# Kernel optimization log

Measured on AMD Instinct MI355X. Metric: run time of the kernel, lower is better.

Reference implementation:

```python
import jax, jax.numpy as jnp
import numpy as np

TEMP = 1.0  # composition softmax temperature

def _bank_topk(x, U, V, logits, top_k):
    # softmax over primitive logits, select top-k, renormalize, fused low-rank projection
    w = jax.nn.softmax(logits / TEMP)                     # [P]
    tw, ti = jax.lax.top_k(w, top_k)                      # [k], [k]
    tw = tw / tw.sum()
    Us = U[ti]                                            # [k, d_in, r]
    Vs = V[ti]                                            # [k, r, d_out]
    h = jnp.einsum('bsd,kdr->bksr', x, Us)                # low-rank bottleneck
    return jnp.einsum('bksr,kro,k->bso', h, Vs, tw)       # weighted fuse

def reference(x, q_U, q_V, k_U, k_V, v_U, v_V, q_logits, k_logits, v_logits, out_w, top_k):
    B, S, _ = x.shape
    H, D = 16, 64
    q = _bank_topk(x, q_U, q_V, q_logits, top_k)
    k = _bank_topk(x, k_U, k_V, k_logits, top_k)
    v = _bank_topk(x, v_U, v_V, v_logits, top_k)
    q = q.reshape(B, S, H, D).transpose(0, 2, 1, 3)       # [B,H,S,D]
    k = k.reshape(B, S, H, D).transpose(0, 2, 1, 3)
    v = v.reshape(B, S, H, D).transpose(0, 2, 1, 3)
    scale = 1.0 / jnp.sqrt(jnp.asarray(D, dtype=x.dtype))
    scores = jnp.einsum('bhqd,bhkd->bhqk', q, k) * scale  # [B,H,S,S]
    causal = jnp.triu(jnp.ones((S, S), dtype=bool), 1)
    scores = jnp.where(causal[None, None], jnp.finfo(x.dtype).min, scores)
    probs = jax.nn.softmax(scores, axis=-1)
    out = jnp.einsum('bhqk,bhkd->bhqd', probs, v)
    out = out.transpose(0, 2, 1, 3).reshape(B, S, H * D)
    return out @ out_w.T                                   # nn.Linear(H*D, d_model, bias=False)

def setup_inputs() -> dict:
    key = jax.random.key(0)
    ks = jax.random.split(key, 11)
    P, d, r = 16, 1024, 64
    B, S = 4, 1024
    f = jnp.float32
    inp = {
        'x': jax.random.normal(ks[0], (B, S, d), f),
        'q_U': jax.random.normal(ks[1], (P, d, r), f) * (1.0 / np.sqrt(d)),
        'q_V': jax.random.normal(ks[2], (P, r, d), f) * (1.0 / np.sqrt(r)),
        'k_U': jax.random.normal(ks[3], (P, d, r), f) * (1.0 / np.sqrt(d)),
        'k_V': jax.random.normal(ks[4], (P, r, d), f) * (1.0 / np.sqrt(r)),
        'v_U': jax.random.normal(ks[5], (P, d, r), f) * (1.0 / np.sqrt(d)),
        'v_V': jax.random.normal(ks[6], (P, r, d), f) * (1.0 / np.sqrt(r)),
        'q_logits': jax.random.normal(ks[7], (P,), f) * 0.01,
        'k_logits': jax.random.normal(ks[8], (P,), f) * 0.01,
        'v_logits': jax.random.normal(ks[9], (P,), f) * 0.01,
        'out_w': jax.random.normal(ks[10], (d, d), f) * (1.0 / np.sqrt(d)),
        'top_k': 4,
    }
    return inp
```

## Files before the change

kernel.cpp:

```cpp
#include <hip/hip_runtime.h>
#include <math.h>

#define D_MODEL 1024
#define RANK    64
#define PMAX    16
#define S_LEN   1024
#define HD      64
#define MROWS   4096
#define NHEAD   16
#define BATCH   4
#define KCMAX   (PMAX * RANK)

typedef short short8v __attribute__((ext_vector_type(8)));
typedef float floatx4 __attribute__((ext_vector_type(4)));

typedef __attribute__((address_space(1))) const unsigned int* gptr_t;
typedef __attribute__((address_space(3))) unsigned int* lptr_t;

static __device__ __forceinline__ void async16(const void* g, void* l) {
    __builtin_amdgcn_global_load_lds((gptr_t)g, (lptr_t)l, 16, 0, 0);
}

static __device__ __forceinline__ short f2bf(float f) {
    unsigned int u = __float_as_uint(f);
    u = (u + 0x7fffu + ((u >> 16) & 1u)) >> 16;
    return (short)u;
}

__global__ void topk_weights_kernel(const float* __restrict__ ql,
                                    const float* __restrict__ kl,
                                    const float* __restrict__ vl,
                                    const int* __restrict__ topk,
                                    int* __restrict__ idx_out,
                                    float* __restrict__ w_out) {
    int bank = threadIdx.x;
    if (bank >= 3) return;
    const float* lg = (bank == 0) ? ql : (bank == 1) ? kl : vl;
    int K = *topk; if (K < 1) K = 1; if (K > PMAX) K = PMAX;
    float l[PMAX];
    for (int i = 0; i < PMAX; ++i) l[i] = lg[i];
    bool used[PMAX];
    for (int i = 0; i < PMAX; ++i) used[i] = false;
    int   sel_i[PMAX];
    float sel_l[PMAX];
    for (int j = 0; j < K; ++j) {
        int best = -1; float bv = -INFINITY;
        for (int i = 0; i < PMAX; ++i)
            if (!used[i] && l[i] > bv) { bv = l[i]; best = i; }
        used[best] = true; sel_i[j] = best; sel_l[j] = bv;
    }
    float mx = sel_l[0];
    float e[PMAX];
    float sum = 0.f;
    for (int j = 0; j < K; ++j) { e[j] = __expf(sel_l[j] - mx); sum += e[j]; }
    float inv = 1.f / sum;
    for (int j = 0; j < PMAX; ++j) {
        idx_out[bank * PMAX + j] = (j < K) ? sel_i[j] : 0;
        w_out[bank * PMAX + j]   = (j < K) ? e[j] * inv : 0.f;
    }
}

__global__ __launch_bounds__(256) void convert_bf16_kernel(
    const float* __restrict__ src, short* __restrict__ dst, int n4) {
    int i = blockIdx.x * 256 + threadIdx.x;
    if (i < n4) {
        float4 f = ((const float4*)src)[i];
        short4 o;
        o.x = f2bf(f.x); o.y = f2bf(f.y); o.z = f2bf(f.z); o.w = f2bf(f.w);
        ((short4*)dst)[i] = o;
    }
}

__global__ __launch_bounds__(256) void prep_uv_kernel(
    const float* __restrict__ qU, const float* __restrict__ kU,
    const float* __restrict__ vU,
    const float* __restrict__ qV, const float* __restrict__ kV,
    const float* __restrict__ vV,
    const int* __restrict__ idx, const float* __restrict__ wsel,
    const int* __restrict__ topk,
    short* __restrict__ Uc, short* __restrict__ Vt) {
    int z    = blockIdx.z;
    int j    = blockIdx.y;
    int tile = blockIdx.x;
    int t    = threadIdx.x;
    int K = *topk; if (K < 1) K = 1; if (K > PMAX) K = PMAX;
    if (j >= K) return;
    __shared__ float T[64][65];
    int bank = (z < 3) ? z : z - 3;
    int p = idx[bank * PMAX + j];

    if (z < 3) {
        const float* U = (bank == 0) ? qU : (bank == 1) ? kU : vU;
        const float* src = U + (size_t)p * D_MODEL * RANK;
        short* dst = Uc + (size_t)bank * D_MODEL * KCMAX;
        int r4 = (t & 15) * 4;
        int dl = t >> 4;
#pragma unroll
        for (int i = 0; i < 4; ++i) {
            int d = tile * 64 + i * 16 + dl;
            float4 f = *(const float4*)&src[(size_t)d * RANK + r4];
            short4 o;
            o.x = f2bf(f.x); o.y = f2bf(f.y); o.z = f2bf(f.z); o.w = f2bf(f.w);
            *(short4*)&dst[(size_t)d * KCMAX + j * 64 + r4] = o;
        }
    } else {
        const float* V = (bank == 0) ? qV : (bank == 1) ? kV : vV;
        float wj = wsel[bank * PMAX + j];
        const float* src = V + (size_t)p * RANK * D_MODEL;
        int n0 = tile * 64;
        int nl = t & 63, rq = t >> 6;
#pragma unroll
        for (int i = 0; i < 16; ++i) {
            int rl = i * 4 + rq;
            T[nl][rl] = src[(size_t)rl * D_MODEL + n0 + nl] * wj;
        }
        __syncthreads();
        short* dst = Vt + (size_t)bank * D_MODEL * KCMAX;
        int rr = t >> 2;
#pragma unroll
        for (int i = 0; i < 4; ++i) {
            int c = (t & 3) * 16 + i * 4;
            short4 o;
            o.x = f2bf(T[rr][c + 0]); o.y = f2bf(T[rr][c + 1]);
            o.z = f2bf(T[rr][c + 2]); o.w = f2bf(T[rr][c + 3]);
            *(short4*)&dst[(size_t)(n0 + rr) * KCMAX + j * 64 + c] = o;
        }
    }
}

static __device__ __forceinline__ void mfma_gemm_tile(
    const short* __restrict__ A, const short* __restrict__ B, int kl,
    int lda, int ldb, int m0, int n0, short* As, short* Bs, floatx4 acc[4][4]) {
    const int t    = threadIdx.x;
    const int w    = t >> 6;
    const int lane = t & 63;
    const int wm   = w & 1, wn = w >> 1;
    const int colL = lane & 15, quad = lane >> 4;
    const int srow  = lane >> 2;
    const int skoff = (lane & 3) * 8;

#pragma unroll
    for (int i = 0; i < 4; ++i)
#pragma unroll
        for (int j = 0; j < 4; ++j) acc[i][j] = (floatx4){0.f, 0.f, 0.f, 0.f};

    for (int k0 = 0; k0 < kl; k0 += 32) {
        async16(A + (size_t)(m0 + w * 16 + srow) * lda + k0 + skoff,
                As + (w * 16 + srow) * 32 + skoff);
        async16(A + (size_t)(m0 + 64 + w * 16 + srow) * lda + k0 + skoff,
                As + (64 + w * 16 + srow) * 32 + skoff);
        async16(B + (size_t)(n0 + w * 16 + srow) * ldb + k0 + skoff,
                Bs + (w * 16 + srow) * 32 + skoff);
        async16(B + (size_t)(n0 + 64 + w * 16 + srow) * ldb + k0 + skoff,
                Bs + (64 + w * 16 + srow) * 32 + skoff);
        __syncthreads();
        short8v af[4], bf[4];
#pragma unroll
        for (int i = 0; i < 4; ++i)
            af[i] = *(const short8v*)&As[(wm * 64 + i * 16 + colL) * 32 + quad * 8];
#pragma unroll
        for (int j = 0; j < 4; ++j)
            bf[j] = *(const short8v*)&Bs[(wn * 64 + j * 16 + colL) * 32 + quad * 8];
#pragma unroll
        for (int i = 0; i < 4; ++i)
#pragma unroll
            for (int j = 0; j < 4; ++j)
                acc[i][j] = __builtin_amdgcn_mfma_f32_16x16x32_bf16(af[i], bf[j], acc[i][j], 0, 0, 0);
        __syncthreads();
    }
}

__global__ __launch_bounds__(256) void gemm_weff_kernel(
    const short* __restrict__ Vt, const short* __restrict__ Uc,
    const int* __restrict__ topk, short* __restrict__ Wt) {
    int K = *topk; if (K < 1) K = 1; if (K > PMAX) K = PMAX;
    int id = blockIdx.x + 8 * (blockIdx.y + 8 * blockIdx.z);
    int sw = (id & 7) * 24 + (id >> 3);
    int m0 = (sw & 7) * 128; int rest = sw >> 3;
    int n0 = (rest & 7) * 128; int bank = rest >> 3;
    __shared__ short As[128 * 32];
    __shared__ short Bs[128 * 32];
    floatx4 acc[4][4];
    mfma_gemm_tile(Vt + (size_t)bank * D_MODEL * KCMAX,
                   Uc + (size_t)bank * D_MODEL * KCMAX,
                   K * 64, KCMAX, KCMAX, m0, n0, As, Bs, acc);

    const int t = threadIdx.x, w = t >> 6, lane = t & 63;
    const int wm = w & 1, wn = w >> 1, colL = lane & 15, quad = lane >> 4;
    short* Wb = Wt + (size_t)bank * D_MODEL * D_MODEL;
#pragma unroll
    for (int i = 0; i < 4; ++i)
#pragma unroll
        for (int j = 0; j < 4; ++j)
#pragma unroll
            for (int r = 0; r < 4; ++r)
                Wb[(size_t)(m0 + wm * 64 + i * 16 + quad * 4 + r) * D_MODEL +
                   (n0 + wn * 64 + j * 16 + colL)] = f2bf(acc[i][j][r]);
}

__global__ __launch_bounds__(256) void gemm_qkv_kernel(
    const short* __restrict__ xb, const short* __restrict__ Wt,
    short* __restrict__ qkv) {
    int id = blockIdx.x + 32 * (blockIdx.y + 8 * blockIdx.z);
    int sw = (id & 7) * 96 + (id >> 3);
    int m0 = (sw & 31) * 128; int rest = sw >> 5;
    int n0 = (rest & 7) * 128; int bank = rest >> 3;
    __shared__ short As[128 * 32];
    __shared__ short Bs[128 * 32];
    floatx4 acc[4][4];
    mfma_gemm_tile(xb, Wt + (size_t)bank * D_MODEL * D_MODEL,
                   D_MODEL, D_MODEL, D_MODEL, m0, n0, As, Bs, acc);

    const int t = threadIdx.x, w = t >> 6, lane = t & 63;
    const int wm = w & 1, wn = w >> 1, colL = lane & 15, quad = lane >> 4;
    short* outp = qkv + (size_t)bank * MROWS * D_MODEL;
#pragma unroll
    for (int i = 0; i < 4; ++i)
#pragma unroll
        for (int j = 0; j < 4; ++j)
#pragma unroll
            for (int r = 0; r < 4; ++r) {
                int m = m0 + wm * 64 + i * 16 + quad * 4 + r;
                int n = n0 + wn * 64 + j * 16 + colL;
                int b = m >> 10, s = m & 1023;
                int head = n >> 6, d = n & 63;
                outp[(((size_t)(b * NHEAD + head) << 10) + s) * HD + d] = f2bf(acc[i][j][r]);
            }
}

__global__ __launch_bounds__(256) void gemm_proj_kernel(
    const short* __restrict__ attnb, const short* __restrict__ wb,
    float* __restrict__ outp) {
    int id = blockIdx.x + 32 * blockIdx.y;
    int sw = (id & 7) * 32 + (id >> 3);
    int m0 = (sw & 31) * 128;
    int n0 = (sw >> 5) * 128;
    __shared__ short As[128 * 32];
    __shared__ short Bs[128 * 32];
    floatx4 acc[4][4];
    mfma_gemm_tile(attnb, wb, D_MODEL, D_MODEL, D_MODEL, m0, n0, As, Bs, acc);

    const int t = threadIdx.x, w = t >> 6, lane = t & 63;
    const int wm = w & 1, wn = w >> 1, colL = lane & 15, quad = lane >> 4;
#pragma unroll
    for (int i = 0; i < 4; ++i)
#pragma unroll
        for (int j = 0; j < 4; ++j)
#pragma unroll
            for (int r = 0; r < 4; ++r)
                outp[(size_t)(m0 + wm * 64 + i * 16 + quad * 4 + r) * D_MODEL +
                     (n0 + wn * 64 + j * 16 + colL)] = acc[i][j][r];
}

__global__ __launch_bounds__(256) void attn_mfma_kernel(
    const short* __restrict__ qkv,
    short* __restrict__ attn_out) {
    const int t    = threadIdx.x;
    const int w    = t >> 6;
    const int lane = t & 63;
    const int col  = lane & 15;
    const int quad = lane >> 4;
    int id = blockIdx.x + 8 * blockIdx.y;
    int sw = (id & 7) * 64 + (id >> 3);
    const int pr = sw & 7;
    const int bh = sw >> 3;
    const size_t HS   = (size_t)S_LEN * HD;
    const size_t BSTR = (size_t)MROWS * D_MODEL;
    const short* Qg = qkv + (size_t)bh * HS;
    const short* Kg = qkv + BSTR + (size_t)bh * HS;
    const short* Vg = qkv + 2 * BSTR + (size_t)bh * HS;

    __shared__ short Ks[128][72];
    __shared__ short Vt[64][136];
    __shared__ short Ps[4][16][136];

    const float SC = 0.125f * 1.44269504f;

    for (int ph = 0; ph < 2; ++ph) {
        const int qt = ph ? (15 - pr) : pr;
        const int qb = qt * 4 + w;
        const int qrow = qt * 64 + w * 16 + col;
        short8v aq0 = *(const short8v*)(Qg + (size_t)qrow * HD + quad * 8);
        short8v aq1 = *(const short8v*)(Qg + (size_t)qrow * HD + 32 + quad * 8);
        floatx4 O0 = {0.f, 0.f, 0.f, 0.f}, O1 = O0, O2 = O0, O3 = O0;
        float mrow[4] = {-INFINITY, -INFINITY, -INFINITY, -INFINITY};
        float lrow[4] = {0.f, 0.f, 0.f, 0.f};
        const int nkv = (qt + 2) >> 1;

        for (int jt = 0; jt < nkv; ++jt) {
            __syncthreads();
#pragma unroll
            for (int it = 0; it < 4; ++it) {
                int idx = t + it * 256;
                int key = idx >> 3, db = (idx & 7) * 8;
                *(short8v*)&Ks[key][db] =
                    *(const short8v*)(Kg + (size_t)(jt * 128 + key) * HD + db);
            }
#pragma unroll
            for (int it = 0; it < 2; ++it) {
                int idx = t + it * 256;
                int k0 = (idx & 63) * 2;
                int db = (idx >> 6) * 8;
                short8v v0 = *(const short8v*)(Vg + (size_t)(jt * 128 + k0) * HD + db);
                short8v v1 = *(const short8v*)(Vg + (size_t)(jt * 128 + k0 + 1) * HD + db);
#pragma unroll
                for (int i = 0; i < 8; ++i) {
                    unsigned int pk = (unsigned int)(unsigned short)v0[i] |
                                      ((unsigned int)(unsigned short)v1[i] << 16);
                    *(unsigned int*)&Vt[db + i][k0] = pk;
                }
            }
            __syncthreads();

            float sc[8][4];
            const int base = jt * 8;
#pragma unroll
            for (int n = 0; n < 8; ++n) {
                int rel = qb - (base + n);
                if (rel >= 0) {
                    floatx4 c4 = {0.f, 0.f, 0.f, 0.f};
                    short8v b0 = *(const short8v*)&Ks[n * 16 + col][quad * 8];
                    short8v b1 = *(const short8v*)&Ks[n * 16 + col][32 + quad * 8];
                    c4 = __builtin_amdgcn_mfma_f32_16x16x32_bf16(aq0, b0, c4, 0, 0, 0);
                    c4 = __builtin_amdgcn_mfma_f32_16x16x32_bf16(aq1, b1, c4, 0, 0, 0);
#pragma unroll
                    for (int r = 0; r < 4; ++r) {
                        float v = c4[r] * SC;
                        if (rel == 0 && col > quad * 4 + r) v = -INFINITY;
                        sc[n][r] = v;
                    }
                } else {
#pragma unroll
                    for (int r = 0; r < 4; ++r) sc[n][r] = -INFINITY;
                }
            }
#pragma unroll
            for (int r = 0; r < 4; ++r) {
                float tm = sc[0][r];
#pragma unroll
                for (int n = 1; n < 8; ++n) tm = fmaxf(tm, sc[n][r]);
                tm = fmaxf(tm, __shfl_xor(tm, 1));
                tm = fmaxf(tm, __shfl_xor(tm, 2));
                tm = fmaxf(tm, __shfl_xor(tm, 4));
                tm = fmaxf(tm, __shfl_xor(tm, 8));
                if (__any(tm > mrow[r] + 8.0f)) {
                    float mnew  = fmaxf(mrow[r], tm);
                    float alpha = exp2f(mrow[r] - mnew);
                    lrow[r] *= alpha;
                    O0[r] *= alpha; O1[r] *= alpha; O2[r] *= alpha; O3[r] *= alpha;
                    mrow[r] = mnew;
                }
                float ps = 0.f;
#pragma unroll
                for (int n = 0; n < 8; ++n) {
                    float p = exp2f(sc[n][r] - mrow[r]);
                    ps += p;
                    Ps[w][quad * 4 + r][n * 16 + col] = f2bf(p);
                }
                ps += __shfl_xor(ps, 1);
                ps += __shfl_xor(ps, 2);
                ps += __shfl_xor(ps, 4);
                ps += __shfl_xor(ps, 8);
                lrow[r] += ps;
            }
            int lim = qb * 16 + 15 - (jt << 7);
            int ksm = lim >> 5; if (ksm > 3) ksm = 3;
#pragma unroll
            for (int ks = 0; ks < 4; ++ks) {
                if (ks > ksm) break;
                short8v ap  = *(const short8v*)&Ps[w][col][ks * 32 + quad * 8];
                short8v bv0 = *(const short8v*)&Vt[0  + col][ks * 32 + quad * 8];
                short8v bv1 = *(const short8v*)&Vt[16 + col][ks * 32 + quad * 8];
                short8v bv2 = *(const short8v*)&Vt[32 + col][ks * 32 + quad * 8];
                short8v bv3 = *(const short8v*)&Vt[48 + col][ks * 32 + quad * 8];
                O0 = __builtin_amdgcn_mfma_f32_16x16x32_bf16(ap, bv0, O0, 0, 0, 0);
                O1 = __builtin_amdgcn_mfma_f32_16x16x32_bf16(ap, bv1, O1, 0, 0, 0);
                O2 = __builtin_amdgcn_mfma_f32_16x16x32_bf16(ap, bv2, O2, 0, 0, 0);
                O3 = __builtin_amdgcn_mfma_f32_16x16x32_bf16(ap, bv3, O3, 0, 0, 0);
            }
        }
        const int b  = bh >> 4;
        const int hh = bh & 15;
        short* orow = attn_out +
            ((size_t)(b * S_LEN) + qt * 64 + w * 16) * D_MODEL + hh * 64;
#pragma unroll
        for (int r = 0; r < 4; ++r) {
            float inv = 1.f / lrow[r];
            short* prw = orow + (size_t)(quad * 4 + r) * D_MODEL;
            prw[0  + col] = f2bf(O0[r] * inv);
            prw[16 + col] = f2bf(O1[r] * inv);
            prw[32 + col] = f2bf(O2[r] * inv);
            prw[48 + col] = f2bf(O3[r] * inv);
        }
    }
}

extern "C" void kernel_launch(void* const* d_in, const int* in_sizes, int n_in,
                              void* d_out, int out_size, void* d_ws, size_t ws_size,
                              hipStream_t stream) {
    const float* x    = (const float*)d_in[0];
    const float* qU   = (const float*)d_in[1];
    const float* qV   = (const float*)d_in[2];
    const float* kU   = (const float*)d_in[3];
    const float* kV   = (const float*)d_in[4];
    const float* vU   = (const float*)d_in[5];
    const float* vV   = (const float*)d_in[6];
    const float* qlg  = (const float*)d_in[7];
    const float* klg  = (const float*)d_in[8];
    const float* vlg  = (const float*)d_in[9];
    const float* outw = (const float*)d_in[10];
    const int*   topk = (const int*)d_in[11];
    float* outp = (float*)d_out;

    char* ws = (char*)d_ws;
    int*   idxp = (int*)ws;
    float* wp   = (float*)(ws + 256);
    short* xb   = (short*)(ws + 512);
    short* Uc   = xb + (size_t)MROWS * D_MODEL;
    short* Vt   = Uc + (size_t)3 * D_MODEL * KCMAX;
    short* wb   = Vt + (size_t)3 * D_MODEL * KCMAX;
    short* Wt   = wb + (size_t)D_MODEL * D_MODEL;
    short* qkvb = Wt + (size_t)3 * D_MODEL * D_MODEL;
    short* attnb = qkvb + (size_t)3 * MROWS * D_MODEL;

    topk_weights_kernel<<<1, 64, 0, stream>>>(qlg, klg, vlg, topk, idxp, wp);
    convert_bf16_kernel<<<(MROWS * D_MODEL / 4 + 255) / 256, 256, 0, stream>>>(
        x, xb, MROWS * D_MODEL / 4);
    convert_bf16_kernel<<<(D_MODEL * D_MODEL / 4 + 255) / 256, 256, 0, stream>>>(
        outw, wb, D_MODEL * D_MODEL / 4);
    prep_uv_kernel<<<dim3(16, 16, 6), 256, 0, stream>>>(
        qU, kU, vU, qV, kV, vV, idxp, wp, topk, Uc, Vt);
    gemm_weff_kernel<<<dim3(8, 8, 3), 256, 0, stream>>>(Vt, Uc, topk, Wt);
    gemm_qkv_kernel<<<dim3(32, 8, 3), 256, 0, stream>>>(xb, Wt, qkvb);
    attn_mfma_kernel<<<dim3(8, 64), 256, 0, stream>>>(qkvb, attnb);
    gemm_proj_kernel<<<dim3(32, 8), 256, 0, stream>>>(attnb, wb, outp);
}
```

Baseline: 222.8 us.

## Restructure attention kernel with transposed S, async LDS loads, and transpose reads

The attention kernel now computes S^T (keys as MFMA rows), so the softmax probabilities already sit in registers in the layout needed as the A operand for the PV product, removing the Ps LDS round-trip. K and V tiles are loaded with global_load_lds async copies into swizzled layouts, and V is read with ds_read_b64_tr_b16 transpose reads instead of being transposed manually by scalar LDS stores. Row statistics become per-lane scalars, reduced across quads and broadcast with shuffles. This trades more complex indexing and inline asm waits for fewer LDS writes and less VALU work.

Measured after the change: 211.9 us. 4.9% less time.

```diff
diff --git a/kernel.cpp b/kernel.cpp
--- a/kernel.cpp
+++ b/kernel.cpp
@@ -12,10 +12,12 @@
 #define KCMAX   (PMAX * RANK)
 
 typedef short short8v __attribute__((ext_vector_type(8)));
+typedef short short4v __attribute__((ext_vector_type(4)));
 typedef float floatx4 __attribute__((ext_vector_type(4)));
 
 typedef __attribute__((address_space(1))) const unsigned int* gptr_t;
 typedef __attribute__((address_space(3))) unsigned int* lptr_t;
+typedef __attribute__((address_space(3))) short* lds3s;
 
 static __device__ __forceinline__ void async16(const void* g, void* l) {
     __builtin_amdgcn_global_load_lds((gptr_t)g, (lptr_t)l, 16, 0, 0);
@@ -261,20 +263,33 @@
     const int col  = lane & 15;
     const int quad = lane >> 4;
     int id = blockIdx.x + 8 * blockIdx.y;
-    int sw = (id & 7) * 64 + (id >> 3);
-    const int pr = sw & 7;
-    const int bh = sw >> 3;
+    int swz = (id & 7) * 64 + (id >> 3);
+    const int pr = swz & 7;
+    const int bh = swz >> 3;
     const size_t HS   = (size_t)S_LEN * HD;
     const size_t BSTR = (size_t)MROWS * D_MODEL;
     const short* Qg = qkv + (size_t)bh * HS;
     const short* Kg = qkv + BSTR + (size_t)bh * HS;
     const short* Vg = qkv + 2 * BSTR + (size_t)bh * HS;
 
-    __shared__ short Ks[128][72];
-    __shared__ short Vt[64][136];
-    __shared__ short Ps[4][16][136];
+    __shared__ short Ks[128 * 64];
+    __shared__ short Vs[128 * 64];
 
     const float SC = 0.125f * 1.44269504f;
+
+    int krow[4], kslot[4], vkey[4], voff[4];
+#pragma unroll
+    for (int it = 0; it < 4; ++it) {
+        int c = t + it * 256;
+        krow[it]  = c >> 3;
+        kslot[it] = (c & 7) ^ ((c >> 3) & 7);
+        int h = c & 1, kr = (c >> 1) & 3, k4 = (c >> 3) & 31, d16 = c >> 8;
+        vkey[it] = k4 * 4 + kr;
+        voff[it] = d16 * 16 + h * 8;
+    }
+    const int sw0 = (quad ^ (col & 7)) * 16;
+    const int sw1 = ((4 + quad) ^ (col & 7)) * 16;
+    lds3s vb = (lds3s)&Vs[quad * 64 + col * 4];
 
     for (int ph = 0; ph < 2; ++ph) {
         const int qt = ph ? (15 - pr) : pr;
@@ -283,109 +298,115 @@
         short8v aq0 = *(const short8v*)(Qg + (size_t)qrow * HD + quad * 8);
         short8v aq1 = *(const short8v*)(Qg + (size_t)qrow * HD + 32 + quad * 8);
         floatx4 O0 = {0.f, 0.f, 0.f, 0.f}, O1 = O0, O2 = O0, O3 = O0;
-        float mrow[4] = {-INFINITY, -INFINITY, -INFINITY, -INFINITY};
-        float lrow[4] = {0.f, 0.f, 0.f, 0.f};
+        float mrow = -INFINITY, lrow = 0.f;
         const int nkv = (qt + 2) >> 1;
 
         for (int jt = 0; jt < nkv; ++jt) {
             __syncthreads();
 #pragma unroll
             for (int it = 0; it < 4; ++it) {
-                int idx = t + it * 256;
-                int key = idx >> 3, db = (idx & 7) * 8;
-                *(short8v*)&Ks[key][db] =
-                    *(const short8v*)(Kg + (size_t)(jt * 128 + key) * HD + db);
+                async16(Kg + (size_t)(jt * 128 + krow[it]) * HD + kslot[it] * 8,
+                        Ks + (t + it * 256) * 8);
+                async16(Vg + (size_t)(jt * 128 + vkey[it]) * HD + voff[it],
+                        Vs + (t + it * 256) * 8);
             }
-#pragma unroll
-            for (int it = 0; it < 2; ++it) {
-                int idx = t + it * 256;
-                int k0 = (idx & 63) * 2;
-                int db = (idx >> 6) * 8;
-                short8v v0 = *(const short8v*)(Vg + (size_t)(jt * 128 + k0) * HD + db);
-                short8v v1 = *(const short8v*)(Vg + (size_t)(jt * 128 + k0 + 1) * HD + db);
-#pragma unroll
-                for (int i = 0; i < 8; ++i) {
-                    unsigned int pk = (unsigned int)(unsigned short)v0[i] |
-                                      ((unsigned int)(unsigned short)v1[i] << 16);
-                    *(unsigned int*)&Vt[db + i][k0] = pk;
+            __syncthreads();
+
+            const int base = jt * 8;
+            float s[8][4];
+#pragma unroll
+            for (int mb = 0; mb < 8; ++mb) {
+                int rel = qb - (base + mb);
+                if (rel >= 0) {
+                    floatx4 c4 = {0.f, 0.f, 0.f, 0.f};
+                    const char* kp = (const char*)Ks + mb * 2048 + col * 128;
+                    short8v a0 = *(const short8v*)(kp + sw0);
+                    short8v a1 = *(const short8v*)(kp + sw1);
+                    c4 = __builtin_amdgcn_mfma_f32_16x16x32_bf16(a0, aq0, c4, 0, 0, 0);
+                    c4 = __builtin_amdgcn_mfma_f32_16x16x32_bf16(a1, aq1, c4, 0, 0, 0);
+#pragma unroll
+                    for (int r = 0; r < 4; ++r) {
+                        float v = c4[r] * SC;
+                        if (rel == 0 && quad * 4 + r > col) v = -INFINITY;
+                        s[mb][r] = v;
+                    }
+                } else {
+#pragma unroll
+                    for (int r = 0; r < 4; ++r) s[mb][r] = -INFINITY;
                 }
             }
-            __syncthreads();
-
-            float sc[8][4];
-            const int base = jt * 8;
-#pragma unroll
-            for (int n = 0; n < 8; ++n) {
-                int rel = qb - (base + n);
-                if (rel >= 0) {
-                    floatx4 c4 = {0.f, 0.f, 0.f, 0.f};
-                    short8v b0 = *(const short8v*)&Ks[n * 16 + col][quad * 8];
-                    short8v b1 = *(const short8v*)&Ks[n * 16 + col][32 + quad * 8];
-                    c4 = __builtin_amdgcn_mfma_f32_16x16x32_bf16(aq0, b0, c4, 0, 0, 0);
-                    c4 = __builtin_amdgcn_mfma_f32_16x16x32_bf16(aq1, b1, c4, 0, 0, 0);
-#pragma unroll
-                    for (int r = 0; r < 4; ++r) {
-                        float v = c4[r] * SC;
-                        if (rel == 0 && col > quad * 4 + r) v = -INFINITY;
-                        sc[n][r] = v;
-                    }
-                } else {
-#pragma unroll
-                    for (int r = 0; r < 4; ++r) sc[n][r] = -INFINITY;
+            float tm = -INFINITY;
+#pragma unroll
+            for (int mb = 0; mb < 8; ++mb)
+#pragma unroll
+                for (int r = 0; r < 4; ++r) tm = fmaxf(tm, s[mb][r]);
+            tm = fmaxf(tm, __shfl_xor(tm, 16));
+            tm = fmaxf(tm, __shfl_xor(tm, 32));
+            if (__any(tm > mrow + 8.0f)) {
+                float mnew  = fmaxf(mrow, tm);
+                float alpha = exp2f(mrow - mnew);
+                lrow *= alpha;
+                mrow = mnew;
+#pragma unroll
+                for (int r = 0; r < 4; ++r) {
+                    float ar = __shfl(alpha, quad * 4 + r);
+                    O0[r] *= ar; O1[r] *= ar; O2[r] *= ar; O3[r] *= ar;
                 }
             }
-#pragma unroll
-            for (int r = 0; r < 4; ++r) {
-                float tm = sc[0][r];
-#pragma unroll
-                for (int n = 1; n < 8; ++n) tm = fmaxf(tm, sc[n][r]);
-                tm = fmaxf(tm, __shfl_xor(tm, 1));
-                tm = fmaxf(tm, __shfl_xor(tm, 2));
-                tm = fmaxf(tm, __shfl_xor(tm, 4));
-                tm = fmaxf(tm, __shfl_xor(tm, 8));
-                if (__any(tm > mrow[r] + 8.0f)) {
-                    float mnew  = fmaxf(mrow[r], tm);
-                    float alpha = exp2f(mrow[r] - mnew);
-                    lrow[r] *= alpha;
-                    O0[r] *= alpha; O1[r] *= alpha; O2[r] *= alpha; O3[r] *= alpha;
-                    mrow[r] = mnew;
+            float p[8][4];
+            float ps = 0.f;
+#pragma unroll
+            for (int mb = 0; mb < 8; ++mb)
+#pragma unroll
+                for (int r = 0; r < 4; ++r) {
+                    float e = exp2f(s[mb][r] - mrow);
+                    p[mb][r] = e; ps += e;
                 }
-                float ps = 0.f;
-#pragma unroll
-                for (int n = 0; n < 8; ++n) {
-                    float p = exp2f(sc[n][r] - mrow[r]);
-                    ps += p;
-                    Ps[w][quad * 4 + r][n * 16 + col] = f2bf(p);
-                }
-                ps += __shfl_xor(ps, 1);
-                ps += __shfl_xor(ps, 2);
-                ps += __shfl_xor(ps, 4);
-                ps += __shfl_xor(ps, 8);
-                lrow[r] += ps;
-            }
+            ps += __shfl_xor(ps, 16);
+            ps += __shfl_xor(ps, 32);
+            lrow += ps;
+
             int lim = qb * 16 + 15 - (jt << 7);
             int ksm = lim >> 5; if (ksm > 3) ksm = 3;
 #pragma unroll
             for (int ks = 0; ks < 4; ++ks) {
-                if (ks > ksm) break;
-                short8v ap  = *(const short8v*)&Ps[w][col][ks * 32 + quad * 8];
-                short8v bv0 = *(const short8v*)&Vt[0  + col][ks * 32 + quad * 8];
-                short8v bv1 = *(const short8v*)&Vt[16 + col][ks * 32 + quad * 8];
-                short8v bv2 = *(const short8v*)&Vt[32 + col][ks * 32 + quad * 8];
-                short8v bv3 = *(const short8v*)&Vt[48 + col][ks * 32 + quad * 8];
-                O0 = __builtin_amdgcn_mfma_f32_16x16x32_bf16(ap, bv0, O0, 0, 0, 0);
-                O1 = __builtin_amdgcn_mfma_f32_16x16x32_bf16(ap, bv1, O1, 0, 0, 0);
-                O2 = __builtin_amdgcn_mfma_f32_16x16x32_bf16(ap, bv2, O2, 0, 0, 0);
-                O3 = __builtin_amdgcn_mfma_f32_16x16x32_bf16(ap, bv3, O3, 0, 0, 0);
+                if (ks <= ksm) {
+                    lds3s vc = vb + ks * 512;
+                    short4v t00, t01, t10, t11, t20, t21, t30, t31;
+                    asm volatile("ds_read_b64_tr_b16 %0, %1" : "=v"(t00) : "v"(vc));
+                    asm volatile("ds_read_b64_tr_b16 %0, %1" : "=v"(t01) : "v"(vc + 256));
+                    asm volatile("ds_read_b64_tr_b16 %0, %1" : "=v"(t10) : "v"(vc + 2048));
+                    asm volatile("ds_read_b64_tr_b16 %0, %1" : "=v"(t11) : "v"(vc + 2304));
+                    asm volatile("ds_read_b64_tr_b16 %0, %1" : "=v"(t20) : "v"(vc + 4096));
+                    asm volatile("ds_read_b64_tr_b16 %0, %1" : "=v"(t21) : "v"(vc + 4352));
+                    asm volatile("ds_read_b64_tr_b16 %0, %1" : "=v"(t30) : "v"(vc + 6144));
+                    asm volatile("ds_read_b64_tr_b16 %0, %1" : "=v"(t31) : "v"(vc + 6400));
+                    short8v ap;
+                    ap[0] = f2bf(p[2 * ks][0]);     ap[1] = f2bf(p[2 * ks][1]);
+                    ap[2] = f2bf(p[2 * ks][2]);     ap[3] = f2bf(p[2 * ks][3]);
+                    ap[4] = f2bf(p[2 * ks + 1][0]); ap[5] = f2bf(p[2 * ks + 1][1]);
+                    ap[6] = f2bf(p[2 * ks + 1][2]); ap[7] = f2bf(p[2 * ks + 1][3]);
+                    asm volatile("s_waitcnt lgkmcnt(0)" ::: "memory");
+                    __builtin_amdgcn_sched_barrier(0);
+                    short8v bv0 = __builtin_shufflevector(t00, t01, 0, 1, 2, 3, 4, 5, 6, 7);
+                    short8v bv1 = __builtin_shufflevector(t10, t11, 0, 1, 2, 3, 4, 5, 6, 7);
+                    short8v bv2 = __builtin_shufflevector(t20, t21, 0, 1, 2, 3, 4, 5, 6, 7);
+                    short8v bv3 = __builtin_shufflevector(t30, t31, 0, 1, 2, 3, 4, 5, 6, 7);
+                    O0 = __builtin_amdgcn_mfma_f32_16x16x32_bf16(ap, bv0, O0, 0, 0, 0);
+                    O1 = __builtin_amdgcn_mfma_f32_16x16x32_bf16(ap, bv1, O1, 0, 0, 0);
+                    O2 = __builtin_amdgcn_mfma_f32_16x16x32_bf16(ap, bv2, O2, 0, 0, 0);
+                    O3 = __builtin_amdgcn_mfma_f32_16x16x32_bf16(ap, bv3, O3, 0, 0, 0);
+                }
             }
         }
         const int b  = bh >> 4;
         const int hh = bh & 15;
         short* orow = attn_out +
             ((size_t)(b * S_LEN) + qt * 64 + w * 16) * D_MODEL + hh * 64;
+        float linv = 1.f / lrow;
 #pragma unroll
         for (int r = 0; r < 4; ++r) {
-            float inv = 1.f / lrow[r];
+            float inv = __shfl(linv, quad * 4 + r);
             short* prw = orow + (size_t)(quad * 4 + r) * D_MODEL;
             prw[0  + col] = f2bf(O0[r] * inv);
             prw[16 + col] = f2bf(O1[r] * inv);
```
